# Performance work log

Hardware: AMD Instinct MI355X
Metric: run time of the kernel (lower is better)

## Reference

```python
import jax, jax.numpy as jnp
import numpy as np

N_QUBITS = 14
N_LAYERS = 2          # n_ansatz_layers
N_TIMESTEPS = 4
DEGREE = 2
N_ROTS = 4 * N_QUBITS * N_LAYERS  # 448 rotation params per qnode call
DIM = 2 ** N_QUBITS
BSZ = 256
STATE_DIM = 4
OUT_DIM = 2


def apply_ry(state, wire, theta):
    # state: (B, 2^n) complex64; theta: (B,) float. Wire 0 = most significant bit (PennyLane convention).
    L, R = 2 ** wire, 2 ** (N_QUBITS - wire - 1)
    st = state.reshape(-1, L, 2, R)
    c = jnp.cos(theta * 0.5)[:, None, None]
    s = jnp.sin(theta * 0.5)[:, None, None]
    s0, s1 = st[:, :, 0, :], st[:, :, 1, :]
    new = jnp.stack([c * s0 - s * s1, s * s0 + c * s1], axis=2)
    return new.reshape(state.shape)


def apply_crx(state, ctrl, tgt, theta):
    # Controlled-RX: RX(theta) on tgt when ctrl bit is 1.
    a, b = (ctrl, tgt) if ctrl < tgt else (tgt, ctrl)
    La, Lm, Lr = 2 ** a, 2 ** (b - a - 1), 2 ** (N_QUBITS - b - 1)
    st = state.reshape(-1, La, 2, Lm, 2, Lr)
    c = jnp.cos(theta * 0.5)[:, None, None, None]
    s = jnp.sin(theta * 0.5)[:, None, None, None]
    if ctrl < tgt:
        # axis2 = ctrl, axis4 = tgt
        ctl1 = st[:, :, 1]                      # (B, La, Lm, 2, Lr)
        t0, t1 = ctl1[:, :, :, 0, :], ctl1[:, :, :, 1, :]
        n0 = c * t0 - 1j * s * t1
        n1 = -1j * s * t0 + c * t1
        new_ctl1 = jnp.stack([n0, n1], axis=3)
        out = jnp.stack([st[:, :, 0], new_ctl1], axis=2)
    else:
        # axis2 = tgt, axis4 = ctrl
        t0c1, t1c1 = st[:, :, 0, :, 1, :], st[:, :, 1, :, 1, :]
        n0 = c * t0c1 - 1j * s * t1c1
        n1 = -1j * s * t0c1 + c * t1c1
        new_t0 = jnp.stack([st[:, :, 0, :, 0, :], n0], axis=3)
        new_t1 = jnp.stack([st[:, :, 1, :, 0, :], n1], axis=3)
        out = jnp.stack([new_t0, new_t1], axis=2)
    return out.reshape(state.shape)


def sim14(state, params):
    # sim14_circuit: per layer -> RY ring, descending CRX ring [i,(i+1)%n], RY ring, CRX ring [i,(i-1)%n].
    idx = 0
    for _ in range(N_LAYERS):
        for i in range(N_QUBITS):
            state = apply_ry(state, i, params[:, idx]); idx += 1
        for i in range(N_QUBITS - 1, -1, -1):
            state = apply_crx(state, i, (i + 1) % N_QUBITS, params[:, idx]); idx += 1
        for i in range(N_QUBITS):
            state = apply_ry(state, i, params[:, idx]); idx += 1
        for i in [N_QUBITS - 1] + list(range(N_QUBITS - 1)):
            state = apply_crx(state, i, (i - 1) % N_QUBITS, params[:, idx]); idx += 1
    return state


def poly_state(base, tparams, mix_coeffs, poly_coeffs):
    # evaluate_polynomial_state_pl: degree+1 rounds of timestep-mixed circuit outputs.
    result = jnp.zeros_like(base)
    for d in range(DEGREE + 1):
        mixed = jnp.zeros_like(base)
        for t in range(N_TIMESTEPS):
            mixed = mixed + mix_coeffs[:, t:t + 1] * sim14(base, tparams[:, t, :])
        result = result + poly_coeffs[d] * mixed
        if d < DEGREE:
            nrm = jnp.linalg.norm(mixed, axis=1, keepdims=True)
            base = mixed / (nrm + 1e-9)
    return result


def expval_z(state, wire):
    L, R = 2 ** wire, 2 ** (N_QUBITS - wire - 1)
    st = state.reshape(-1, L, 2, R)
    p = jnp.sum(jnp.abs(st) ** 2, axis=(1, 3))  # (B, 2)
    return p[:, 0] - p[:, 1]


def setup_inputs() -> dict:
    key = jax.random.key(0)
    ks = jax.random.split(key, 7)
    return {
        "x": jax.random.normal(ks[0], (BSZ, STATE_DIM), dtype=jnp.float32),
        "W_in": jax.random.normal(ks[1], (STATE_DIM, N_TIMESTEPS * N_ROTS), dtype=jnp.float32) * 0.3,
        "b_in": jax.random.normal(ks[2], (N_TIMESTEPS * N_ROTS,), dtype=jnp.float32) * 0.1,
        "mix_coeffs": jax.random.normal(ks[3], (1, N_TIMESTEPS), dtype=jnp.float32) * 0.5,
        "poly_coeffs": jax.random.normal(ks[4], (DEGREE + 1,), dtype=jnp.float32) * 0.5,
        "W_out": jax.random.normal(ks[5], (N_QUBITS, OUT_DIM), dtype=jnp.float32) * 0.3,
        "b_out": jax.random.normal(ks[6], (OUT_DIM,), dtype=jnp.float32) * 0.1,
    }


def reference(x, W_in, b_in, mix_coeffs, poly_coeffs, W_out, b_out):
    bsz = x.shape[0]
    # v1-style sigmoid [0,1] angle scaling
    angles = jax.nn.sigmoid(x @ W_in + b_in)                # (B, T*n_rots)
    tparams = angles.reshape(bsz, N_TIMESTEPS, N_ROTS)
    base = jnp.zeros((bsz, DIM), dtype=jnp.complex64).at[:, 0].set(1.0)
    final = poly_state(base, tparams, mix_coeffs, poly_coeffs)
    final = final / (jnp.linalg.norm(final, axis=1, keepdims=True) + 1e-9)
    expz = jnp.stack([expval_z(final, w) for w in range(N_QUBITS)], axis=1)  # (B, n_qubits) real
    return expz.astype(jnp.float32) @ W_out + b_out
```

## Files before the change

### kernel.cpp

```cpp
#include <hip/hip_runtime.h>
#include <math.h>

#define DIM 16384
#define NTH 512

typedef float v2f __attribute__((ext_vector_type(2)));

__host__ __device__ constexpr int cswz(int i) {
  return i ^ ((i >> 4) & 15) ^ ((i >> 8) & 15) ^ ((i >> 12) & 3);
}

constexpr int LW[8][5] = {
  {13, 12, 11, 10, 0},
  {10, 9, 8, 7, 6},
  {6, 5, 4, 3, 2},
  {2, 1, 0, 3, 4},
  {12, 13, 0, 1, 2},
  {2, 3, 4, 5, 6},
  {6, 7, 8, 9, 10},
  {10, 11, 12, 13, 9},
};
constexpr int PMAP[8][9] = {
  {4, 5, 6, 7, 8, 9, 10, 11, 12},
  {0, 1, 2, 11, 8, 9, 10, 12, 13},
  {0, 1, 2, 3, 4, 5, 6, 12, 13},
  {0, 1, 2, 3, 4, 5, 6, 7, 8},
  {2, 3, 4, 5, 6, 7, 8, 9, 10},
  {0, 1, 2, 3, 4, 5, 6, 12, 13},
  {0, 1, 2, 11, 8, 9, 10, 12, 13},
  {5, 6, 7, 8, 9, 10, 11, 12, 13},
};
constexpr int NG[8] = {9, 8, 8, 3, 9, 8, 8, 3};
constexpr int GATES[8][9][4] = {
  {{0,4,0,0},{0,3,0,10},{0,2,0,11},{0,1,0,12},{0,0,0,13},{1,0,4,14},{1,1,0,15},{1,2,1,16},{1,3,2,17}},
  {{0,4,0,6},{0,3,0,7},{0,2,0,8},{0,1,0,9},{1,1,0,18},{1,2,1,19},{1,3,2,20},{1,4,3,21},{0,0,0,0}},
  {{0,4,0,2},{0,3,0,3},{0,2,0,4},{0,1,0,5},{1,1,0,22},{1,2,1,23},{1,3,2,24},{1,4,3,25},{0,0,0,0}},
  {{0,1,0,1},{1,1,0,26},{1,2,1,27},{0,0,0,0},{0,0,0,0},{0,0,0,0},{0,0,0,0},{0,0,0,0},{0,0,0,0}},
  {{0,2,0,28},{0,3,0,29},{0,4,0,30},{0,0,0,40},{0,1,0,41},{1,1,0,42},{1,2,1,43},{1,3,2,44},{1,4,3,45}},
  {{0,1,0,31},{0,2,0,32},{0,3,0,33},{0,4,0,34},{1,1,0,46},{1,2,1,47},{1,3,2,48},{1,4,3,49},{0,0,0,0}},
  {{0,1,0,35},{0,2,0,36},{0,3,0,37},{0,4,0,38},{1,1,0,50},{1,2,1,51},{1,3,2,52},{1,4,3,53},{0,0,0,0}},
  {{0,1,0,39},{1,1,0,54},{1,2,1,55},{0,0,0,0},{0,0,0,0},{0,0,0,0},{0,0,0,0},{0,0,0,0},{0,0,0,0}},
};

__host__ __device__ constexpr int offcube(int p, int j) {
  int o = 0;
  for (int b = 0; b < 5; ++b)
    if ((j >> b) & 1) o |= 1 << (13 - LW[p][b]);
  return o;
}

template <int PID, int MODE>
__device__ __forceinline__ void run_pass(v2f* __restrict__ S, const v2f* __restrict__ CS,
                                         int lb, int tid, v2f* __restrict__ a) {
  int base = 0;
#pragma unroll
  for (int k = 0; k < 9; ++k) base |= ((tid >> k) & 1) << PMAP[PID][k];
  const int sb = cswz(base);
  if (MODE == 1) {
#pragma unroll
    for (int j = 0; j < 32; ++j) a[j] = v2f{0.f, 0.f};
    if (tid == 0) a[0] = v2f{1.f, 0.f};
  } else {
#pragma unroll
    for (int j = 0; j < 32; ++j) a[j] = S[sb ^ cswz(offcube(PID, j))];
  }
#pragma unroll
  for (int g = 0; g < NG[PID]; ++g) {
    const v2f cs2 = CS[lb + GATES[PID][g][3]];
    const float c = cs2.x, s = cs2.y;
    if (GATES[PID][g][0] == 0) {
      const int tb = GATES[PID][g][1];
#pragma unroll
      for (int j = 0; j < 32; ++j)
        if (!((j >> tb) & 1)) {
          const int j2 = j | (1 << tb);
          const v2f a0 = a[j], a1 = a[j2];
          a[j]  = c * a0 - s * a1;
          a[j2] = s * a0 + c * a1;
        }
    } else {
      const int bc = GATES[PID][g][1], bt = GATES[PID][g][2];
#pragma unroll
      for (int j = 0; j < 32; ++j)
        if (((j >> bc) & 1) && !((j >> bt) & 1)) {
          const int j2 = j | (1 << bt);
          const v2f t0 = a[j], t1 = a[j2];
          a[j]  = c * t0 + s * v2f{t1.y, -t1.x};
          a[j2] = c * t1 + s * v2f{t0.y, -t0.x};
        }
    }
  }
  if (MODE != 2) {
#pragma unroll
    for (int j = 0; j < 32; ++j) S[sb ^ cswz(offcube(PID, j))] = a[j];
  }
  __syncthreads();
}

__device__ __forceinline__ void run_sim(v2f* __restrict__ S, const v2f* __restrict__ CS,
                                        int tid, v2f* __restrict__ a,
                                        const v2f* __restrict__ basev, int own_sb,
                                        bool initzero) {
  if (initzero) {
    run_pass<0, 1>(S, CS, 0, tid, a);
  } else {
#pragma unroll
    for (int j = 0; j < 32; ++j) S[own_sb ^ cswz(offcube(7, j))] = basev[j];
    __syncthreads();
    run_pass<0, 0>(S, CS, 0, tid, a);
  }
  run_pass<1, 0>(S, CS, 0, tid, a);
  run_pass<2, 0>(S, CS, 0, tid, a);
  run_pass<3, 0>(S, CS, 0, tid, a);
  run_pass<4, 0>(S, CS, 0, tid, a);
  run_pass<5, 0>(S, CS, 0, tid, a);
  run_pass<6, 0>(S, CS, 0, tid, a);
  run_pass<7, 0>(S, CS, 0, tid, a);
  run_pass<0, 0>(S, CS, 56, tid, a);
  run_pass<1, 0>(S, CS, 56, tid, a);
  run_pass<2, 0>(S, CS, 56, tid, a);
  run_pass<3, 0>(S, CS, 56, tid, a);
  run_pass<4, 0>(S, CS, 56, tid, a);
  run_pass<5, 0>(S, CS, 56, tid, a);
  run_pass<6, 0>(S, CS, 56, tid, a);
  run_pass<7, 2>(S, CS, 56, tid, a);
}

__device__ __forceinline__ float block_sum(float v, int tid, float* red) {
#pragma unroll
  for (int off = 32; off; off >>= 1) v += __shfl_xor(v, off);
  if ((tid & 63) == 0) red[tid >> 6] = v;
  __syncthreads();
  float tot = 0.f;
#pragma unroll
  for (int w = 0; w < 8; ++w) tot += red[w];
  __syncthreads();
  return tot;
}

__global__ __launch_bounds__(NTH, 1) void qts_kernel(
    const float* __restrict__ x, const float* __restrict__ Win,
    const float* __restrict__ bin, const float* __restrict__ mix,
    const float* __restrict__ poly, const float* __restrict__ Wout,
    const float* __restrict__ bout, float* __restrict__ out) {
  __shared__ v2f S[DIM + 448 + 128];
  v2f* CSall = S + DIM;
  float* red = (float*)(S + DIM + 448);
  const int tid = threadIdx.x;
  const int b = blockIdx.x;

  if (tid < 448) {
    float z = bin[tid];
    const float x0 = x[b * 4 + 0], x1 = x[b * 4 + 1], x2 = x[b * 4 + 2], x3 = x[b * 4 + 3];
    z += x0 * Win[tid] + x1 * Win[448 + tid] + x2 * Win[896 + tid] + x3 * Win[1344 + tid];
    const float th = 1.f / (1.f + expf(-z));
    float sn, cc;
    sincosf(0.5f * th, &sn, &cc);
    CSall[tid] = v2f{cc, sn};
  }
  __syncthreads();

  int ownbase = 0;
#pragma unroll
  for (int k = 0; k < 9; ++k) ownbase |= ((tid >> k) & 1) << PMAP[7][k];
  const int own_sb = cswz(ownbase);

  const float p0 = poly[0], p1 = poly[1], p2 = poly[2];

  v2f a[32], acc[32], basev[32];
  float alpha;

#pragma unroll
  for (int j = 0; j < 32; ++j) acc[j] = v2f{0.f, 0.f};
  for (int t = 0; t < 4; ++t) {
    run_sim(S, CSall + t * 112, tid, a, basev, own_sb, true);
    const float mc = mix[t];
#pragma unroll
    for (int j = 0; j < 32; ++j) acc[j] += mc * a[j];
  }
  {
    float part = 0.f;
#pragma unroll
    for (int j = 0; j < 32; ++j) part += acc[j].x * acc[j].x + acc[j].y * acc[j].y;
    const float tot = block_sum(part, tid, red);
    const float nu = sqrtf(tot) + 1e-9f;
    const float inv = 1.f / nu;
    alpha = p0 * nu;
#pragma unroll
    for (int j = 0; j < 32; ++j) { basev[j] = inv * acc[j]; acc[j] = v2f{0.f, 0.f}; }
  }

  for (int t = 0; t < 4; ++t) {
    run_sim(S, CSall + t * 112, tid, a, basev, own_sb, false);
    const float mc = mix[t];
#pragma unroll
    for (int j = 0; j < 32; ++j) acc[j] += mc * a[j];
  }
  {
    float part = 0.f;
#pragma unroll
    for (int j = 0; j < 32; ++j) part += acc[j].x * acc[j].x + acc[j].y * acc[j].y;
    const float tot = block_sum(part, tid, red);
    const float nu = sqrtf(tot) + 1e-9f;
    const float inv = 1.f / nu;
#pragma unroll
    for (int j = 0; j < 32; ++j) {
      const v2f tmp = acc[j];
      acc[j] = alpha * basev[j] + p1 * tmp;
      basev[j] = inv * tmp;
    }
  }

  for (int t = 0; t < 4; ++t) {
    run_sim(S, CSall + t * 112, tid, a, basev, own_sb, false);
    const float mc = p2 * mix[t];
#pragma unroll
    for (int j = 0; j < 32; ++j) acc[j] += mc * a[j];
  }

  float part[15];
#pragma unroll
  for (int v = 0; v < 15; ++v) part[v] = 0.f;
#pragma unroll
  for (int j = 0; j < 32; ++j) {
    const int idx = ownbase | offcube(7, j);
    const float p = acc[j].x * acc[j].x + acc[j].y * acc[j].y;
    part[14] += p;
#pragma unroll
    for (int w = 0; w < 14; ++w) part[w] += ((idx >> (13 - w)) & 1) ? -p : p;
  }
  __syncthreads();
#pragma unroll
  for (int v = 0; v < 15; ++v) {
    float xv = part[v];
#pragma unroll
    for (int off = 32; off; off >>= 1) xv += __shfl_xor(xv, off);
    if ((tid & 63) == 0) red[(tid >> 6) * 15 + v] = xv;
  }
  __syncthreads();
  if (tid < 15) {
    float tot = 0.f;
#pragma unroll
    for (int w = 0; w < 8; ++w) tot += red[w * 15 + tid];
    red[128 + tid] = tot;
  }
  __syncthreads();
  if (tid < 2) {
    const float nrm = sqrtf(red[128 + 14]) + 1e-9f;
    const float iv = 1.f / (nrm * nrm);
    float o = bout[tid];
#pragma unroll
    for (int w = 0; w < 14; ++w) o += red[128 + w] * iv * Wout[w * 2 + tid];
    out[b * 2 + tid] = o;
  }
}

extern "C" void kernel_launch(void* const* d_in, const int* in_sizes, int n_in,
                              void* d_out, int out_size, void* d_ws, size_t ws_size,
                              hipStream_t stream) {
  const float* x    = (const float*)d_in[0];
  const float* Win  = (const float*)d_in[1];
  const float* bin  = (const float*)d_in[2];
  const float* mix  = (const float*)d_in[3];
  const float* poly = (const float*)d_in[4];
  const float* Wout = (const float*)d_in[5];
  const float* bout = (const float*)d_in[6];
  float* out = (float*)d_out;

  qts_kernel<<<256, NTH, 0, stream>>>(x, Win, bin, mix, poly, Wout, bout, out);
}
```

Before: 959.2 us.

## Use 4-qubit sub-cubes, fuse mix accumulation, and spill intermediate states to workspace

```diff
diff --git a/kernel.cpp b/kernel.cpp
--- a/kernel.cpp
+++ b/kernel.cpp
@@ -3,6 +3,7 @@
 
 #define DIM 16384
 #define NTH 512
+#define NBLK 256
 
 typedef float v2f __attribute__((ext_vector_type(2)));
 
@@ -10,25 +11,299 @@
   return i ^ ((i >> 4) & 15) ^ ((i >> 8) & 15) ^ ((i >> 12) & 3);
 }
 
+constexpr int LWp[10][4] = {
+  {13, 0, 12, 11},
+  {10, 9, 8, 11},
+  {7, 6, 5, 8},
+  {4, 3, 2, 5},
+  {1, 0, 2, 3},
+  {13, 12, 0, 1},
+  {2, 1, 3, 4},
+  {5, 4, 6, 7},
+  {8, 7, 9, 10},
+  {11, 10, 12, 9},
+};
+constexpr int PM[10][10] = {
+  {3, 4, 5, 6, 7, 8, 9, 10, 11, 12},
+  {0, 1, 6, 7, 8, 9, 10, 11, 12, 13},
+  {0, 1, 2, 3, 4, 9, 10, 11, 12, 13},
+  {0, 1, 2, 3, 4, 5, 6, 7, 12, 13},
+  {0, 1, 2, 3, 4, 5, 6, 7, 8, 9},
+  {2, 3, 4, 5, 6, 7, 8, 9, 10, 11},
+  {0, 1, 2, 3, 4, 5, 6, 7, 8, 13},
+  {0, 1, 2, 3, 4, 5, 10, 11, 12, 13},
+  {0, 1, 2, 7, 8, 9, 10, 11, 12, 13},
+  {0, 5, 6, 7, 8, 9, 10, 11, 12, 13},
+};
+constexpr int NGp[10] = {7, 6, 6, 6, 3, 7, 6, 6, 6, 3};
+constexpr int GT[10][7][4] = {
+  {{0,0,0,13},{0,1,0,0},{0,2,0,12},{0,3,0,11},{1,0,1,14},{1,2,0,15},{1,3,2,16}},
+  {{0,0,0,10},{0,1,0,9},{0,2,0,8},{1,0,3,17},{1,1,0,18},{1,2,1,19},{0,0,0,0}},
+  {{0,0,0,7},{0,1,0,6},{0,2,0,5},{1,0,3,20},{1,1,0,21},{1,2,1,22},{0,0,0,0}},
+  {{0,0,0,4},{0,1,0,3},{0,2,0,2},{1,0,3,23},{1,1,0,24},{1,2,1,25},{0,0,0,0}},
+  {{0,0,0,1},{1,0,2,26},{1,1,0,27},{0,0,0,0},{0,0,0,0},{0,0,0,0},{0,0,0,0}},
+  {{0,0,0,41},{0,1,0,40},{0,2,0,28},{0,3,0,29},{1,0,1,42},{1,2,0,43},{1,3,2,44}},
+  {{0,0,0,30},{0,2,0,31},{0,3,0,32},{1,0,1,45},{1,2,0,46},{1,3,2,47},{0,0,0,0}},
+  {{0,0,0,33},{0,2,0,34},{0,3,0,35},{1,0,1,48},{1,2,0,49},{1,3,2,50},{0,0,0,0}},
+  {{0,0,0,36},{0,2,0,37},{0,3,0,38},{1,0,1,51},{1,2,0,52},{1,3,2,53},{0,0,0,0}},
+  {{0,0,0,39},{1,0,1,54},{1,2,0,55},{0,0,0,0},{0,0,0,0},{0,0,0,0},{0,0,0,0}},
+};
+
+__host__ __device__ constexpr int offcube4(int p, int j) {
+  int o = 0;
+  for (int b = 0; b < 4; ++b)
+    if ((j >> b) & 1) o |= 1 << (13 - LWp[p][b]);
+  return o;
+}
+
+template <int PID>
+__device__ __forceinline__ int sub_slot(int tid, int h) {
+  int base = h << PM[PID][9];
+#pragma unroll
+  for (int k = 0; k < 9; ++k) base |= ((tid >> k) & 1) << PM[PID][k];
+  return cswz(base);
+}
+
+template <int PID>
+__device__ __forceinline__ void gates16(const v2f* __restrict__ CS, v2f* __restrict__ a) {
+#pragma unroll
+  for (int g = 0; g < NGp[PID]; ++g) {
+    const v2f cs2 = CS[GT[PID][g][3]];
+    const float c = cs2.x, s = cs2.y;
+    if (GT[PID][g][0] == 0) {
+      const int tb = GT[PID][g][1];
+#pragma unroll
+      for (int j = 0; j < 16; ++j)
+        if (!((j >> tb) & 1)) {
+          const int j2 = j | (1 << tb);
+          const v2f a0 = a[j], a1 = a[j2];
+          a[j]  = c * a0 - s * a1;
+          a[j2] = s * a0 + c * a1;
+        }
+    } else {
+      const int bc = GT[PID][g][1], bt = GT[PID][g][2];
+#pragma unroll
+      for (int j = 0; j < 16; ++j)
+        if (((j >> bc) & 1) && !((j >> bt) & 1)) {
+          const int j2 = j | (1 << bt);
+          const v2f t0 = a[j], t1 = a[j2];
+          a[j]  = c * t0 + s * v2f{t1.y, -t1.x};
+          a[j2] = c * t1 + s * v2f{t0.y, -t0.x};
+        }
+    }
+  }
+}
+
+template <int PID, int MODE>
+__device__ __forceinline__ void pass2(v2f* __restrict__ S, const v2f* __restrict__ CS,
+                                      int tid, v2f* __restrict__ acc, float mc) {
+#pragma unroll
+  for (int h = 0; h < 2; ++h) {
+    const int sb = sub_slot<PID>(tid, h);
+    v2f a[16];
+    if (MODE == 1) {
+#pragma unroll
+      for (int j = 0; j < 16; ++j) a[j] = v2f{0.f, 0.f};
+      if (tid == 0 && h == 0) a[0] = v2f{1.f, 0.f};
+    } else {
+#pragma unroll
+      for (int j = 0; j < 16; ++j) a[j] = S[sb ^ cswz(offcube4(PID, j))];
+    }
+    gates16<PID>(CS, a);
+    if (MODE == 2) {
+#pragma unroll
+      for (int j = 0; j < 16; ++j) acc[h * 16 + j] += mc * a[j];
+    } else {
+#pragma unroll
+      for (int j = 0; j < 16; ++j) S[sb ^ cswz(offcube4(PID, j))] = a[j];
+    }
+  }
+  __syncthreads();
+}
+
+template <bool INITZERO>
+__device__ __forceinline__ void run_sim(v2f* __restrict__ S, const v2f* __restrict__ CS,
+                                        int tid, v2f* __restrict__ acc, float mc) {
+  if (INITZERO) pass2<0, 1>(S, CS, tid, acc, 0.f);
+  else          pass2<0, 0>(S, CS, tid, acc, 0.f);
+  pass2<1, 0>(S, CS, tid, acc, 0.f);
+  pass2<2, 0>(S, CS, tid, acc, 0.f);
+  pass2<3, 0>(S, CS, tid, acc, 0.f);
+  pass2<4, 0>(S, CS, tid, acc, 0.f);
+  pass2<5, 0>(S, CS, tid, acc, 0.f);
+  pass2<6, 0>(S, CS, tid, acc, 0.f);
+  pass2<7, 0>(S, CS, tid, acc, 0.f);
+  pass2<8, 0>(S, CS, tid, acc, 0.f);
+  pass2<9, 0>(S, CS, tid, acc, 0.f);
+  const v2f* C2 = CS + 56;
+  pass2<0, 0>(S, C2, tid, acc, 0.f);
+  pass2<1, 0>(S, C2, tid, acc, 0.f);
+  pass2<2, 0>(S, C2, tid, acc, 0.f);
+  pass2<3, 0>(S, C2, tid, acc, 0.f);
+  pass2<4, 0>(S, C2, tid, acc, 0.f);
+  pass2<5, 0>(S, C2, tid, acc, 0.f);
+  pass2<6, 0>(S, C2, tid, acc, 0.f);
+  pass2<7, 0>(S, C2, tid, acc, 0.f);
+  pass2<8, 0>(S, C2, tid, acc, 0.f);
+  pass2<9, 2>(S, C2, tid, acc, mc);
+}
+
+__device__ __forceinline__ void export_state(v2f* __restrict__ S, v2f* __restrict__ g,
+                                             int tid, const v2f* __restrict__ acc) {
+#pragma unroll
+  for (int h = 0; h < 2; ++h) {
+    const int sb = sub_slot<9>(tid, h);
+#pragma unroll
+    for (int j = 0; j < 16; ++j) S[sb ^ cswz(offcube4(9, j))] = acc[h * 16 + j];
+  }
+  __syncthreads();
+#pragma unroll
+  for (int j = 0; j < 32; ++j) { const int s = tid + j * NTH; g[s] = S[s]; }
+  __syncthreads();
+}
+
+__device__ __forceinline__ float block_sum(float v, int tid, float* red) {
+#pragma unroll
+  for (int off = 32; off; off >>= 1) v += __shfl_xor(v, off);
+  if ((tid & 63) == 0) red[tid >> 6] = v;
+  __syncthreads();
+  float tot = 0.f;
+#pragma unroll
+  for (int w = 0; w < 8; ++w) tot += red[w];
+  __syncthreads();
+  return tot;
+}
+
+__global__ __launch_bounds__(NTH, 1) void qts_kernel(
+    const float* __restrict__ x, const float* __restrict__ Win,
+    const float* __restrict__ bin, const float* __restrict__ mix,
+    const float* __restrict__ poly, const float* __restrict__ Wout,
+    const float* __restrict__ bout, float* __restrict__ out,
+    v2f* __restrict__ gAall, v2f* __restrict__ gBall) {
+  __shared__ v2f S[DIM + 448 + 128];
+  v2f* CSall = S + DIM;
+  float* red = (float*)(S + DIM + 448);
+  const int tid = threadIdx.x;
+  const int b = blockIdx.x;
+  v2f* gA = gAall + (size_t)b * DIM;
+  v2f* gB = gBall + (size_t)b * DIM;
+
+  if (tid < 448) {
+    float z = bin[tid];
+    const float x0 = x[b * 4 + 0], x1 = x[b * 4 + 1], x2 = x[b * 4 + 2], x3 = x[b * 4 + 3];
+    z += x0 * Win[tid] + x1 * Win[448 + tid] + x2 * Win[896 + tid] + x3 * Win[1344 + tid];
+    const float th = 1.f / (1.f + expf(-z));
+    float sn, cc;
+    sincosf(0.5f * th, &sn, &cc);
+    CSall[tid] = v2f{cc, sn};
+  }
+  __syncthreads();
+
+  const float p0 = poly[0], p1 = poly[1], p2 = poly[2];
+  v2f acc[32];
+
+#pragma unroll
+  for (int j = 0; j < 32; ++j) acc[j] = v2f{0.f, 0.f};
+  for (int t = 0; t < 4; ++t)
+    run_sim<true>(S, CSall + t * 112, tid, acc, mix[t]);
+  float n1;
+  {
+    float part = 0.f;
+#pragma unroll
+    for (int j = 0; j < 32; ++j) part += acc[j].x * acc[j].x + acc[j].y * acc[j].y;
+    n1 = sqrtf(block_sum(part, tid, red));
+  }
+  export_state(S, gA, tid, acc);
+
+#pragma unroll
+  for (int j = 0; j < 32; ++j) acc[j] = v2f{0.f, 0.f};
+  for (int t = 0; t < 4; ++t) {
+    if (t) {
+#pragma unroll
+      for (int j = 0; j < 32; ++j) { const int s = tid + j * NTH; S[s] = gA[s]; }
+      __syncthreads();
+    }
+    run_sim<false>(S, CSall + t * 112, tid, acc, mix[t]);
+  }
+  float n2;
+  {
+    float part = 0.f;
+#pragma unroll
+    for (int j = 0; j < 32; ++j) part += acc[j].x * acc[j].x + acc[j].y * acc[j].y;
+    n2 = sqrtf(block_sum(part, tid, red));
+  }
+  export_state(S, gB, tid, acc);
+
+#pragma unroll
+  for (int j = 0; j < 32; ++j) acc[j] = v2f{0.f, 0.f};
+  for (int t = 0; t < 4; ++t) {
+    if (t) {
+#pragma unroll
+      for (int j = 0; j < 32; ++j) { const int s = tid + j * NTH; S[s] = gB[s]; }
+      __syncthreads();
+    }
+    run_sim<false>(S, CSall + t * 112, tid, acc, mix[t]);
+  }
+#pragma unroll
+  for (int h = 0; h < 2; ++h) {
+    const int sb = sub_slot<9>(tid, h);
+#pragma unroll
+    for (int j = 0; j < 16; ++j) S[sb ^ cswz(offcube4(9, j))] = acc[h * 16 + j];
+  }
+  __syncthreads();
+
+  const float n1e = n1 + 1e-9f;
+  const float n2e = n2 + 1e-9f * n1e;
+  const float c2 = p1 / n1e;
+  const float c3 = p2 / n2e;
+  float part[15];
+#pragma unroll
+  for (int v = 0; v < 15; ++v) part[v] = 0.f;
+#pragma unroll
+  for (int j = 0; j < 32; ++j) {
+    const int s = tid + j * NTH;
+    const int i = cswz(s);
+    const v2f r = p0 * gA[s] + c2 * gB[s] + c3 * S[s];
+    const float p = r.x * r.x + r.y * r.y;
+    part[14] += p;
+#pragma unroll
+    for (int w = 0; w < 14; ++w) part[w] += ((i >> (13 - w)) & 1) ? -p : p;
+  }
+  __syncthreads();
+#pragma unroll
+  for (int v = 0; v < 15; ++v) {
+    float xv = part[v];
+#pragma unroll
+    for (int off = 32; off; off >>= 1) xv += __shfl_xor(xv, off);
+    if ((tid & 63) == 0) red[(tid >> 6) * 15 + v] = xv;
+  }
+  __syncthreads();
+  if (tid < 15) {
+    float tot = 0.f;
+#pragma unroll
+    for (int w = 0; w < 8; ++w) tot += red[w * 15 + tid];
+    red[128 + tid] = tot;
+  }
+  __syncthreads();
+  if (tid < 2) {
+    const float nrm = sqrtf(red[128 + 14]) + 1e-9f;
+    const float iv = 1.f / (nrm * nrm);
+    float o = bout[tid];
+#pragma unroll
+    for (int w = 0; w < 14; ++w) o += red[128 + w] * iv * Wout[w * 2 + tid];
+    out[b * 2 + tid] = o;
+  }
+}
+
 constexpr int LW[8][5] = {
-  {13, 12, 11, 10, 0},
-  {10, 9, 8, 7, 6},
-  {6, 5, 4, 3, 2},
-  {2, 1, 0, 3, 4},
-  {12, 13, 0, 1, 2},
-  {2, 3, 4, 5, 6},
-  {6, 7, 8, 9, 10},
-  {10, 11, 12, 13, 9},
+  {13, 12, 11, 10, 0}, {10, 9, 8, 7, 6}, {6, 5, 4, 3, 2}, {2, 1, 0, 3, 4},
+  {12, 13, 0, 1, 2}, {2, 3, 4, 5, 6}, {6, 7, 8, 9, 10}, {10, 11, 12, 13, 9},
 };
 constexpr int PMAP[8][9] = {
-  {4, 5, 6, 7, 8, 9, 10, 11, 12},
-  {0, 1, 2, 11, 8, 9, 10, 12, 13},
-  {0, 1, 2, 3, 4, 5, 6, 12, 13},
-  {0, 1, 2, 3, 4, 5, 6, 7, 8},
-  {2, 3, 4, 5, 6, 7, 8, 9, 10},
-  {0, 1, 2, 3, 4, 5, 6, 12, 13},
-  {0, 1, 2, 11, 8, 9, 10, 12, 13},
-  {5, 6, 7, 8, 9, 10, 11, 12, 13},
+  {4, 5, 6, 7, 8, 9, 10, 11, 12}, {0, 1, 2, 11, 8, 9, 10, 12, 13},
+  {0, 1, 2, 3, 4, 5, 6, 12, 13}, {0, 1, 2, 3, 4, 5, 6, 7, 8},
+  {2, 3, 4, 5, 6, 7, 8, 9, 10}, {0, 1, 2, 3, 4, 5, 6, 12, 13},
+  {0, 1, 2, 11, 8, 9, 10, 12, 13}, {5, 6, 7, 8, 9, 10, 11, 12, 13},
 };
 constexpr int NG[8] = {9, 8, 8, 3, 9, 8, 8, 3};
 constexpr int GATES[8][9][4] = {
@@ -41,17 +316,15 @@
   {{0,1,0,35},{0,2,0,36},{0,3,0,37},{0,4,0,38},{1,1,0,50},{1,2,1,51},{1,3,2,52},{1,4,3,53},{0,0,0,0}},
   {{0,1,0,39},{1,1,0,54},{1,2,1,55},{0,0,0,0},{0,0,0,0},{0,0,0,0},{0,0,0,0},{0,0,0,0},{0,0,0,0}},
 };
-
-__host__ __device__ constexpr int offcube(int p, int j) {
+__host__ __device__ constexpr int offcube5(int p, int j) {
   int o = 0;
   for (int b = 0; b < 5; ++b)
     if ((j >> b) & 1) o |= 1 << (13 - LW[p][b]);
   return o;
 }
-
 template <int PID, int MODE>
-__device__ __forceinline__ void run_pass(v2f* __restrict__ S, const v2f* __restrict__ CS,
-                                         int lb, int tid, v2f* __restrict__ a) {
+__device__ __forceinline__ void fb_pass(v2f* __restrict__ S, const v2f* __restrict__ CS,
+                                        int lb, int tid, v2f* __restrict__ a) {
   int base = 0;
 #pragma unroll
   for (int k = 0; k < 9; ++k) base |= ((tid >> k) & 1) << PMAP[PID][k];
@@ -62,7 +335,7 @@
     if (tid == 0) a[0] = v2f{1.f, 0.f};
   } else {
 #pragma unroll
-    for (int j = 0; j < 32; ++j) a[j] = S[sb ^ cswz(offcube(PID, j))];
+    for (int j = 0; j < 32; ++j) a[j] = S[sb ^ cswz(offcube5(PID, j))];
   }
 #pragma unroll
   for (int g = 0; g < NG[PID]; ++g) {
@@ -92,53 +365,39 @@
   }
   if (MODE != 2) {
 #pragma unroll
-    for (int j = 0; j < 32; ++j) S[sb ^ cswz(offcube(PID, j))] = a[j];
-  }
-  __syncthreads();
-}
-
-__device__ __forceinline__ void run_sim(v2f* __restrict__ S, const v2f* __restrict__ CS,
-                                        int tid, v2f* __restrict__ a,
-                                        const v2f* __restrict__ basev, int own_sb,
-                                        bool initzero) {
+    for (int j = 0; j < 32; ++j) S[sb ^ cswz(offcube5(PID, j))] = a[j];
+  }
+  __syncthreads();
+}
+__device__ __forceinline__ void fb_sim(v2f* __restrict__ S, const v2f* __restrict__ CS,
+                                       int tid, v2f* __restrict__ a,
+                                       const v2f* __restrict__ basev, int own_sb,
+                                       bool initzero) {
   if (initzero) {
-    run_pass<0, 1>(S, CS, 0, tid, a);
+    fb_pass<0, 1>(S, CS, 0, tid, a);
   } else {
 #pragma unroll
-    for (int j = 0; j < 32; ++j) S[own_sb ^ cswz(offcube(7, j))] = basev[j];
+    for (int j = 0; j < 32; ++j) S[own_sb ^ cswz(offcube5(7, j))] = basev[j];
     __syncthreads();
-    run_pass<0, 0>(S, CS, 0, tid, a);
-  }
-  run_pass<1, 0>(S, CS, 0, tid, a);
-  run_pass<2, 0>(S, CS, 0, tid, a);
-  run_pass<3, 0>(S, CS, 0, tid, a);
-  run_pass<4, 0>(S, CS, 0, tid, a);
-  run_pass<5, 0>(S, CS, 0, tid, a);
-  run_pass<6, 0>(S, CS, 0, tid, a);
-  run_pass<7, 0>(S, CS, 0, tid, a);
-  run_pass<0, 0>(S, CS, 56, tid, a);
-  run_pass<1, 0>(S, CS, 56, tid, a);
-  run_pass<2, 0>(S, CS, 56, tid, a);
-  run_pass<3, 0>(S, CS, 56, tid, a);
-  run_pass<4, 0>(S, CS, 56, tid, a);
-  run_pass<5, 0>(S, CS, 56, tid, a);
-  run_pass<6, 0>(S, CS, 56, tid, a);
-  run_pass<7, 2>(S, CS, 56, tid, a);
-}
-
-__device__ __forceinline__ float block_sum(float v, int tid, float* red) {
-#pragma unroll
-  for (int off = 32; off; off >>= 1) v += __shfl_xor(v, off);
-  if ((tid & 63) == 0) red[tid >> 6] = v;
-  __syncthreads();
-  float tot = 0.f;
-#pragma unroll
-  for (int w = 0; w < 8; ++w) tot += red[w];
-  __syncthreads();
-  return tot;
-}
-
-__global__ __launch_bounds__(NTH, 1) void qts_kernel(
+    fb_pass<0, 0>(S, CS, 0, tid, a);
+  }
+  fb_pass<1, 0>(S, CS, 0, tid, a);
+  fb_pass<2, 0>(S, CS, 0, tid, a);
+  fb_pass<3, 0>(S, CS, 0, tid, a);
+  fb_pass<4, 0>(S, CS, 0, tid, a);
+  fb_pass<5, 0>(S, CS, 0, tid, a);
+  fb_pass<6, 0>(S, CS, 0, tid, a);
+  fb_pass<7, 0>(S, CS, 0, tid, a);
+  fb_pass<0, 0>(S, CS, 56, tid, a);
+  fb_pass<1, 0>(S, CS, 56, tid, a);
+  fb_pass<2, 0>(S, CS, 56, tid, a);
+  fb_pass<3, 0>(S, CS, 56, tid, a);
+  fb_pass<4, 0>(S, CS, 56, tid, a);
+  fb_pass<5, 0>(S, CS, 56, tid, a);
+  fb_pass<6, 0>(S, CS, 56, tid, a);
+  fb_pass<7, 2>(S, CS, 56, tid, a);
+}
+__global__ __launch_bounds__(NTH, 1) void qts_fb(
     const float* __restrict__ x, const float* __restrict__ Win,
     const float* __restrict__ bin, const float* __restrict__ mix,
     const float* __restrict__ poly, const float* __restrict__ Wout,
@@ -148,7 +407,6 @@
   float* red = (float*)(S + DIM + 448);
   const int tid = threadIdx.x;
   const int b = blockIdx.x;
-
   if (tid < 448) {
     float z = bin[tid];
     const float x0 = x[b * 4 + 0], x1 = x[b * 4 + 1], x2 = x[b * 4 + 2], x3 = x[b * 4 + 3];
@@ -159,21 +417,17 @@
     CSall[tid] = v2f{cc, sn};
   }
   __syncthreads();
-
   int ownbase = 0;
 #pragma unroll
   for (int k = 0; k < 9; ++k) ownbase |= ((tid >> k) & 1) << PMAP[7][k];
   const int own_sb = cswz(ownbase);
-
   const float p0 = poly[0], p1 = poly[1], p2 = poly[2];
-
   v2f a[32], acc[32], basev[32];
   float alpha;
-
 #pragma unroll
   for (int j = 0; j < 32; ++j) acc[j] = v2f{0.f, 0.f};
   for (int t = 0; t < 4; ++t) {
-    run_sim(S, CSall + t * 112, tid, a, basev, own_sb, true);
+    fb_sim(S, CSall + t * 112, tid, a, basev, own_sb, true);
     const float mc = mix[t];
 #pragma unroll
     for (int j = 0; j < 32; ++j) acc[j] += mc * a[j];
@@ -189,9 +443,8 @@
 #pragma unroll
     for (int j = 0; j < 32; ++j) { basev[j] = inv * acc[j]; acc[j] = v2f{0.f, 0.f}; }
   }
-
   for (int t = 0; t < 4; ++t) {
-    run_sim(S, CSall + t * 112, tid, a, basev, own_sb, false);
+    fb_sim(S, CSall + t * 112, tid, a, basev, own_sb, false);
     const float mc = mix[t];
 #pragma unroll
     for (int j = 0; j < 32; ++j) acc[j] += mc * a[j];
@@ -210,20 +463,18 @@
       basev[j] = inv * tmp;
     }
   }
-
   for (int t = 0; t < 4; ++t) {
-    run_sim(S, CSall + t * 112, tid, a, basev, own_sb, false);
+    fb_sim(S, CSall + t * 112, tid, a, basev, own_sb, false);
     const float mc = p2 * mix[t];
 #pragma unroll
     for (int j = 0; j < 32; ++j) acc[j] += mc * a[j];
   }
-
   float part[15];
 #pragma unroll
   for (int v = 0; v < 15; ++v) part[v] = 0.f;
 #pragma unroll
   for (int j = 0; j < 32; ++j) {
-    const int idx = ownbase | offcube(7, j);
+    const int idx = ownbase | offcube5(7, j);
     const float p = acc[j].x * acc[j].x + acc[j].y * acc[j].y;
     part[14] += p;
 #pragma unroll
@@ -267,5 +518,12 @@
   const float* bout = (const float*)d_in[6];
   float* out = (float*)d_out;
 
-  qts_kernel<<<256, NTH, 0, stream>>>(x, Win, bin, mix, poly, Wout, bout, out);
-}
+  const size_t need = 2ull * NBLK * DIM * sizeof(float) * 2;
+  if (ws_size >= need) {
+    v2f* gA = (v2f*)d_ws;
+    v2f* gB = gA + (size_t)NBLK * DIM;
+    qts_kernel<<<NBLK, NTH, 0, stream>>>(x, Win, bin, mix, poly, Wout, bout, out, gA, gB);
+  } else {
+    qts_fb<<<NBLK, NTH, 0, stream>>>(x, Win, bin, mix, poly, Wout, bout, out);
+  }
+}
```

Result: slower. 1.605 ms (+67.3%).
